# Kernel optimization log

Hardware: AMD Instinct MI355X
Metric: run time of the kernel (lower is better)

The kernel has to match this reference:

```python
import jax, jax.numpy as jnp
import numpy as np

B, S, D = 8, 2048, 512

def setup_inputs() -> dict:
    key = jax.random.key(0)
    ks = jax.random.split(key, 9)
    scale = 1.0 / np.sqrt(D)
    q = jax.random.normal(ks[0], (B, S, D), dtype=jnp.float32)
    k = jax.random.normal(ks[1], (B, S, D), dtype=jnp.float32)
    v = jax.random.normal(ks[2], (B, S, D), dtype=jnp.float32)
    # causal mask, broadcast over batch: True = attend
    mask = jnp.tril(jnp.ones((S, S), dtype=bool))[None, :, :]
    Wq = jax.random.normal(ks[3], (D, D), dtype=jnp.float32) * scale
    bq = jax.random.normal(ks[4], (D,), dtype=jnp.float32) * scale
    Wk = jax.random.normal(ks[5], (D, D), dtype=jnp.float32) * scale
    bk = jax.random.normal(ks[6], (D,), dtype=jnp.float32) * scale
    Wv = jax.random.normal(ks[7], (D, D), dtype=jnp.float32) * scale
    bv = jax.random.normal(ks[8], (D,), dtype=jnp.float32) * scale
    return {"q": q, "k": k, "v": v, "mask": mask,
            "Wq": Wq, "bq": bq, "Wk": Wk, "bk": bk, "Wv": Wv, "bv": bv}

def reference(q, k, v, mask, Wq, bq, Wk, bk, Wv, bv):
    # torch nn.Linear: x @ W^T + b
    Q = jnp.einsum('bsd,ed->bse', q, Wq) + bq
    K = jnp.einsum('bsd,ed->bse', k, Wk) + bk
    V = jnp.einsum('bsd,ed->bse', v, Wv) + bv
    scores = jnp.einsum('bqd,bkd->bqk', Q, K) / jnp.sqrt(jnp.float32(D))
    scores = jnp.where(mask, scores, jnp.float32(-1e9))
    prob = jax.nn.softmax(scores, axis=-1)
    out = jnp.einsum('bqk,bkd->bqd', prob, V)
    return out
```

## Files before the change

### kernel.cpp

```cpp
#include <hip/hip_runtime.h>
#include <stdint.h>
#include <stddef.h>
#include <math.h>

typedef _Float16 half8 __attribute__((ext_vector_type(8)));
typedef float f32x4 __attribute__((ext_vector_type(4)));

#define SCALE_QK 0.04419417382415922f

__device__ __forceinline__ void gload16(const void* g, void* lds) {
  __builtin_amdgcn_global_load_lds(
      (const __attribute__((address_space(1))) void*)g,
      (__attribute__((address_space(3))) void*)lds,
      16, 0, 0);
}

template<bool A_F32>
__device__ __forceinline__ void run_kloop_sb(const void* Arow0, const _Float16* Brow0,
                                             int lda, int ldb, int kIters,
                                             _Float16* As, _Float16* Bs,
                                             f32x4 (&acc)[4][4])
{
  const int tid  = threadIdx.x;
  const int lane = tid & 63;
  const int w    = tid >> 6;
  const int wm   = w >> 1, wn = w & 1;
  const int srow = tid >> 3;
  const int sg   = tid & 7;
  const int swz  = sg ^ (srow & 7);
  const int fr   = lane & 15;
  const int fq   = lane >> 4;
  const int fx   = lane & 7;

  for (int it = 0; it < kIters; ++it) {
    const int k0 = it * 64;
    if constexpr (A_F32) {
      const float* A = (const float*)Arow0;
      f32x4 preF[8];
      #pragma unroll
      for (int i = 0; i < 4; ++i) {
        const float* src = A + (size_t)(i*32 + srow) * lda + (k0 + sg*8);
        preF[2*i]   = *(const f32x4*)src;
        preF[2*i+1] = *(const f32x4*)(src + 4);
      }
      #pragma unroll
      for (int i = 0; i < 4; ++i)
        gload16(Brow0 + (size_t)(i*32 + srow) * ldb + (k0 + swz*8), Bs + i*2048 + w*512);
      #pragma unroll
      for (int i = 0; i < 4; ++i) {
        f32x4 x = preF[2*i], y = preF[2*i+1];
        half8 h;
        h[0]=(_Float16)x[0]; h[1]=(_Float16)x[1]; h[2]=(_Float16)x[2]; h[3]=(_Float16)x[3];
        h[4]=(_Float16)y[0]; h[5]=(_Float16)y[1]; h[6]=(_Float16)y[2]; h[7]=(_Float16)y[3];
        *(half8*)(As + (i*32 + srow)*64 + swz*8) = h;
      }
    } else {
      const _Float16* A = (const _Float16*)Arow0;
      #pragma unroll
      for (int i = 0; i < 4; ++i)
        gload16(A + (size_t)(i*32 + srow) * lda + (k0 + swz*8), As + i*2048 + w*512);
      #pragma unroll
      for (int i = 0; i < 4; ++i)
        gload16(Brow0 + (size_t)(i*32 + srow) * ldb + (k0 + swz*8), Bs + i*2048 + w*512);
    }
    __syncthreads();

    #pragma unroll
    for (int ks = 0; ks < 2; ++ks) {
      half8 av[4], bv[4];
      const int slot = (ks*4 + fq) ^ fx;
      #pragma unroll
      for (int i = 0; i < 4; ++i) {
        av[i] = *(const half8*)(As + (wm*64 + i*16 + fr)*64 + slot*8);
        bv[i] = *(const half8*)(Bs + (wn*64 + i*16 + fr)*64 + slot*8);
      }
      #pragma unroll
      for (int i = 0; i < 4; ++i) {
        #pragma unroll
        for (int j = 0; j < 4; ++j)
          acc[i][j] = __builtin_amdgcn_mfma_f32_16x16x32_f16(av[i], bv[j], acc[i][j], 0, 0, 0);
      }
    }
    __syncthreads();
  }
}

__global__ __launch_bounds__(256) void k_cvtw(const float* __restrict__ Wq,
                                              const float* __restrict__ Wk,
                                              const float* __restrict__ Wv,
                                              _Float16* __restrict__ Wb)
{
  const int t = blockIdx.x * 256 + threadIdx.x;
  const int base = t * 8;
  const int z = base >> 18;
  const int off = base & 262143;
  const float* src = (z == 0) ? Wq : ((z == 1) ? Wk : Wv);
  f32x4 a = *(const f32x4*)(src + off);
  f32x4 b = *(const f32x4*)(src + off + 4);
  half8 h;
  h[0]=(_Float16)a[0]; h[1]=(_Float16)a[1]; h[2]=(_Float16)a[2]; h[3]=(_Float16)a[3];
  h[4]=(_Float16)b[0]; h[5]=(_Float16)b[1]; h[6]=(_Float16)b[2]; h[7]=(_Float16)b[3];
  *(half8*)(Wb + base) = h;
}

__global__ __launch_bounds__(256, 3) void k_proj(const float* __restrict__ q,
                                                 const float* __restrict__ k,
                                                 const float* __restrict__ v,
                                                 const _Float16* __restrict__ Wb,
                                                 const float* __restrict__ bq,
                                                 const float* __restrict__ bk,
                                                 const float* __restrict__ bv,
                                                 _Float16* __restrict__ Qb,
                                                 _Float16* __restrict__ Kb,
                                                 _Float16* __restrict__ Vt)
{
  __shared__ __align__(16) _Float16 LDSbuf[128*132];
  _Float16* As = LDSbuf;
  _Float16* Bs = LDSbuf + 8192;

  const int bid = blockIdx.x;
  const int xcd = bid & 7, i = bid >> 3;
  const int p = xcd * 48 + (i >> 2);
  const int nt = i & 3;
  const int z = p >> 7, mt = p & 127;

  const float* A     = (z == 0) ? q  : (z == 1) ? k  : v;
  const float* bia   = (z == 0) ? bq : (z == 1) ? bk : bv;
  const _Float16* B  = Wb + (size_t)z * 512 * 512;

  f32x4 acc[4][4] = {};
  run_kloop_sb<true>(A + (size_t)mt*128*512, B + (size_t)nt*128*512, 512, 512, 8,
                     As, Bs, acc);

  const int tid = threadIdx.x;
  const int lane = tid & 63, w = tid >> 6;
  const int wm = w >> 1, wn = w & 1;
  const int fr = lane & 15, fq = lane >> 4;

  if (z < 2) {
    _Float16* C = (z == 0) ? Qb : Kb;
    #pragma unroll
    for (int j = 0; j < 4; ++j) {
      const int col = nt*128 + wn*64 + j*16 + fr;
      const float bval = bia[col];
      #pragma unroll
      for (int i2 = 0; i2 < 4; ++i2) {
        const int row = mt*128 + wm*64 + i2*16 + fq*4;
        #pragma unroll
        for (int r = 0; r < 4; ++r)
          C[(size_t)(row + r) * 512 + col] = (_Float16)(acc[i2][j][r] + bval);
      }
    }
  } else {
    _Float16* sm = LDSbuf;
    #pragma unroll
    for (int j = 0; j < 4; ++j) {
      const int colloc = wn*64 + j*16 + fr;
      const float bval = bia[nt*128 + colloc];
      #pragma unroll
      for (int i2 = 0; i2 < 4; ++i2) {
        const int rowloc = wm*64 + i2*16 + fq*4;
        #pragma unroll
        for (int r = 0; r < 4; ++r)
          sm[colloc*132 + rowloc + r] = (_Float16)(acc[i2][j][r] + bval);
      }
    }
    __syncthreads();
    const int bb = mt >> 4, s0 = (mt & 15) * 128;
    #pragma unroll
    for (int q8 = 0; q8 < 8; ++q8) {
      const int dloc = q8*16 + (tid >> 4);
      const int ch   = tid & 15;
      half8 o = *(const half8*)&sm[dloc*132 + ch*8];
      *(half8*)(Vt + ((size_t)bb*512 + nt*128 + dloc)*2048 + s0 + ch*8) = o;
    }
  }
}

__global__ __launch_bounds__(256, 4) void k_scores(const _Float16* __restrict__ Qb,
                                                   const _Float16* __restrict__ Kb,
                                                   _Float16* __restrict__ P)
{
  __shared__ __align__(16) _Float16 As[128*64], Bs[128*64];
  const int bid = blockIdx.x;
  const int b = bid & 7;
  const int t = bid >> 3;
  int qt = (int)((sqrtf(8.0f * (float)t + 1.0f) - 1.0f) * 0.5f);
  int base = (qt * (qt + 1)) >> 1;
  if (t < base)                { --qt; base = (qt * (qt + 1)) >> 1; }
  else if (t >= base + qt + 1) { ++qt; base = (qt * (qt + 1)) >> 1; }
  const int kt = t - base;

  f32x4 acc[4][4] = {};
  run_kloop_sb<false>(Qb + ((size_t)b*2048 + qt*128)*512,
                      Kb + ((size_t)b*2048 + kt*128)*512,
                      512, 512, 8, As, Bs, acc);
  const int lane = threadIdx.x & 63, w = threadIdx.x >> 6;
  const int wm = w >> 1, wn = w & 1;
  const int fr = lane & 15, fq = lane >> 4;
  #pragma unroll
  for (int i = 0; i < 4; ++i) {
    const int row = qt*128 + wm*64 + i*16 + fq*4;
    #pragma unroll
    for (int j = 0; j < 4; ++j) {
      const int col = kt*128 + wn*64 + j*16 + fr;
      #pragma unroll
      for (int r = 0; r < 4; ++r)
        P[((size_t)b*2048 + row + r) * 2048 + col] = (_Float16)(acc[i][j][r] * SCALE_QK);
    }
  }
}

__global__ __launch_bounds__(256) void k_softmax(_Float16* __restrict__ P)
{
  const int lane = threadIdx.x & 63;
  const int row  = blockIdx.x * 4 + (threadIdx.x >> 6);
  const int qIdx = row & 2047;
  _Float16* p = P + (size_t)row * 2048;
  const int L    = qIdx + 1;
  const int Lpad = ((qIdx >> 7) + 1) * 128;

  half8 xb[4];
  float m = -1e30f, s = 0.f;
  #pragma unroll
  for (int c = 0; c < 4; ++c) {
    const int i0 = lane * 8 + c * 512;
    if (i0 < Lpad) {
      half8 x = *(const half8*)(p + i0);
      xb[c] = x;
      float xv[8];
      #pragma unroll
      for (int j = 0; j < 8; ++j) xv[j] = (i0 + j < L) ? (float)x[j] : -1e30f;
      float cm = xv[0];
      #pragma unroll
      for (int j = 1; j < 8; ++j) cm = fmaxf(cm, xv[j]);
      const float mn = fmaxf(m, cm);
      float cs = 0.f;
      #pragma unroll
      for (int j = 0; j < 8; ++j) cs += __expf(xv[j] - mn);
      s = s * __expf(m - mn) + cs;
      m = mn;
    }
  }
  #pragma unroll
  for (int d = 1; d < 64; d <<= 1) {
    const float mo = __shfl_xor(m, d, 64);
    const float so = __shfl_xor(s, d, 64);
    const float mn = fmaxf(m, mo);
    s = s * __expf(m - mn) + so * __expf(mo - mn);
    m = mn;
  }
  const float inv = 1.0f / s;

  #pragma unroll
  for (int c = 0; c < 4; ++c) {
    const int i0 = lane * 8 + c * 512;
    if (i0 < Lpad) {
      half8 x = xb[c];
      half8 o;
      #pragma unroll
      for (int j = 0; j < 8; ++j)
        o[j] = (i0 + j < L) ? (_Float16)(__expf((float)x[j] - m) * inv) : (_Float16)0.f;
      *(half8*)(p + i0) = o;
    }
  }
}

__global__ __launch_bounds__(256, 4) void k_pv(const _Float16* __restrict__ P,
                                               const _Float16* __restrict__ Vt,
                                               float* __restrict__ Out)
{
  __shared__ __align__(16) _Float16 As[128*64], Bs[128*64];
  const int bid = blockIdx.x;
  const int b = bid & 7;
  const int r0 = bid >> 3;
  const int qi = r0 >> 2, dt = r0 & 3;
  const int qt = (qi & 1) ? (15 - (qi >> 1)) : (qi >> 1);

  f32x4 acc[4][4] = {};
  run_kloop_sb<false>(P  + ((size_t)b*2048 + qt*128)*2048,
                      Vt + ((size_t)b*512  + dt*128)*2048,
                      2048, 2048, (qt + 1) * 2, As, Bs, acc);
  const int lane = threadIdx.x & 63, w = threadIdx.x >> 6;
  const int wm = w >> 1, wn = w & 1;
  const int fr = lane & 15, fq = lane >> 4;
  #pragma unroll
  for (int i = 0; i < 4; ++i) {
    const int row = qt*128 + wm*64 + i*16 + fq*4;
    #pragma unroll
    for (int j = 0; j < 4; ++j) {
      const int col = dt*128 + wn*64 + j*16 + fr;
      #pragma unroll
      for (int r = 0; r < 4; ++r)
        Out[((size_t)b*2048 + row + r) * 512 + col] = acc[i][j][r];
    }
  }
}

extern "C" void kernel_launch(void* const* d_in, const int* in_sizes, int n_in,
                              void* d_out, int out_size, void* d_ws, size_t ws_size,
                              hipStream_t stream) {
  (void)in_sizes; (void)n_in; (void)out_size;
  const float* q  = (const float*)d_in[0];
  const float* k  = (const float*)d_in[1];
  const float* v  = (const float*)d_in[2];
  const float* Wq = (const float*)d_in[4];
  const float* bq = (const float*)d_in[5];
  const float* Wk = (const float*)d_in[6];
  const float* bk = (const float*)d_in[7];
  const float* Wv = (const float*)d_in[8];
  const float* bv = (const float*)d_in[9];

  const size_t OFF_P  = 0;
  const size_t OFF_Q  = (size_t)64 << 20;
  const size_t OFF_K  = (size_t)80 << 20;
  const size_t OFF_VT = (size_t)112 << 20;
  const size_t OFF_W  = (size_t)128 << 20;
  const size_t NEEDED = OFF_W + (size_t)3 * 512 * 512 * sizeof(_Float16);
  if (ws_size < NEEDED) return;

  char* ws = (char*)d_ws;
  _Float16* P  = (_Float16*)(ws + OFF_P);
  _Float16* Qb = (_Float16*)(ws + OFF_Q);
  _Float16* Kb = (_Float16*)(ws + OFF_K);
  _Float16* Vt = (_Float16*)(ws + OFF_VT);
  _Float16* Wb = (_Float16*)(ws + OFF_W);
  float* Out = (float*)d_out;

  k_cvtw   <<<dim3(384),  dim3(256), 0, stream>>>(Wq, Wk, Wv, Wb);
  k_proj   <<<dim3(1536), dim3(256), 0, stream>>>(q, k, v, Wb, bq, bk, bv, Qb, Kb, Vt);
  k_scores <<<dim3(1088), dim3(256), 0, stream>>>(Qb, Kb, P);
  k_softmax<<<dim3(4096), dim3(256), 0, stream>>>(P);
  k_pv     <<<dim3(512),  dim3(256), 0, stream>>>(P, Vt, Out);
}
```

Before: 262.7 us.

## Widen projection and score GEMM tiles to 128x256 with per-wave N=128

After: 270.5 us. +3.0%, slower.

```diff
diff --git a/kernel.cpp b/kernel.cpp
--- a/kernel.cpp
+++ b/kernel.cpp
@@ -16,10 +16,10 @@
 }
 
 template<bool A_F32>
-__device__ __forceinline__ void run_kloop_sb(const void* Arow0, const _Float16* Brow0,
-                                             int lda, int ldb, int kIters,
-                                             _Float16* As, _Float16* Bs,
-                                             f32x4 (&acc)[4][4])
+__device__ __forceinline__ void run_kloop_wide(const void* Arow0, const _Float16* Brow0,
+                                               int lda, int ldb, int kIters,
+                                               _Float16* As, _Float16* Bs,
+                                               f32x4 (&acc)[4][8])
 {
   const int tid  = threadIdx.x;
   const int lane = tid & 63;
@@ -44,7 +44,7 @@
         preF[2*i+1] = *(const f32x4*)(src + 4);
       }
       #pragma unroll
-      for (int i = 0; i < 4; ++i)
+      for (int i = 0; i < 8; ++i)
         gload16(Brow0 + (size_t)(i*32 + srow) * ldb + (k0 + swz*8), Bs + i*2048 + w*512);
       #pragma unroll
       for (int i = 0; i < 4; ++i) {
@@ -60,9 +60,56 @@
       for (int i = 0; i < 4; ++i)
         gload16(A + (size_t)(i*32 + srow) * lda + (k0 + swz*8), As + i*2048 + w*512);
       #pragma unroll
+      for (int i = 0; i < 8; ++i)
+        gload16(Brow0 + (size_t)(i*32 + srow) * ldb + (k0 + swz*8), Bs + i*2048 + w*512);
+    }
+    __syncthreads();
+
+    #pragma unroll
+    for (int ks = 0; ks < 2; ++ks) {
+      half8 av[4], bv[8];
+      const int slot = (ks*4 + fq) ^ fx;
+      #pragma unroll
       for (int i = 0; i < 4; ++i)
-        gload16(Brow0 + (size_t)(i*32 + srow) * ldb + (k0 + swz*8), Bs + i*2048 + w*512);
-    }
+        av[i] = *(const half8*)(As + (wm*64 + i*16 + fr)*64 + slot*8);
+      #pragma unroll
+      for (int j = 0; j < 8; ++j)
+        bv[j] = *(const half8*)(Bs + (wn*128 + j*16 + fr)*64 + slot*8);
+      #pragma unroll
+      for (int i = 0; i < 4; ++i) {
+        #pragma unroll
+        for (int j = 0; j < 8; ++j)
+          acc[i][j] = __builtin_amdgcn_mfma_f32_16x16x32_f16(av[i], bv[j], acc[i][j], 0, 0, 0);
+      }
+    }
+    __syncthreads();
+  }
+}
+
+__device__ __forceinline__ void run_kloop_sb(const _Float16* Arow0, const _Float16* Brow0,
+                                             int lda, int ldb, int kIters,
+                                             _Float16* As, _Float16* Bs,
+                                             f32x4 (&acc)[4][4])
+{
+  const int tid  = threadIdx.x;
+  const int lane = tid & 63;
+  const int w    = tid >> 6;
+  const int wm   = w >> 1, wn = w & 1;
+  const int srow = tid >> 3;
+  const int sg   = tid & 7;
+  const int swz  = sg ^ (srow & 7);
+  const int fr   = lane & 15;
+  const int fq   = lane >> 4;
+  const int fx   = lane & 7;
+
+  for (int it = 0; it < kIters; ++it) {
+    const int k0 = it * 64;
+    #pragma unroll
+    for (int i = 0; i < 4; ++i)
+      gload16(Arow0 + (size_t)(i*32 + srow) * lda + (k0 + swz*8), As + i*2048 + w*512);
+    #pragma unroll
+    for (int i = 0; i < 4; ++i)
+      gload16(Brow0 + (size_t)(i*32 + srow) * ldb + (k0 + swz*8), Bs + i*2048 + w*512);
     __syncthreads();
 
     #pragma unroll
@@ -103,7 +150,7 @@
   *(half8*)(Wb + base) = h;
 }
 
-__global__ __launch_bounds__(256, 3) void k_proj(const float* __restrict__ q,
+__global__ __launch_bounds__(256, 2) void k_proj(const float* __restrict__ q,
                                                  const float* __restrict__ k,
                                                  const float* __restrict__ v,
                                                  const _Float16* __restrict__ Wb,
@@ -114,23 +161,23 @@
                                                  _Float16* __restrict__ Kb,
                                                  _Float16* __restrict__ Vt)
 {
-  __shared__ __align__(16) _Float16 LDSbuf[128*132];
+  __shared__ __align__(16) _Float16 LDSbuf[256*132];
   _Float16* As = LDSbuf;
   _Float16* Bs = LDSbuf + 8192;
 
   const int bid = blockIdx.x;
   const int xcd = bid & 7, i = bid >> 3;
-  const int p = xcd * 48 + (i >> 2);
-  const int nt = i & 3;
+  const int p = xcd * 48 + (i >> 1);
+  const int nt2 = i & 1;
   const int z = p >> 7, mt = p & 127;
 
   const float* A     = (z == 0) ? q  : (z == 1) ? k  : v;
   const float* bia   = (z == 0) ? bq : (z == 1) ? bk : bv;
   const _Float16* B  = Wb + (size_t)z * 512 * 512;
 
-  f32x4 acc[4][4] = {};
-  run_kloop_sb<true>(A + (size_t)mt*128*512, B + (size_t)nt*128*512, 512, 512, 8,
-                     As, Bs, acc);
+  f32x4 acc[4][8] = {};
+  run_kloop_wide<true>(A + (size_t)mt*128*512, B + (size_t)nt2*256*512, 512, 512, 8,
+                       As, Bs, acc);
 
   const int tid = threadIdx.x;
   const int lane = tid & 63, w = tid >> 6;
@@ -140,8 +187,8 @@
   if (z < 2) {
     _Float16* C = (z == 0) ? Qb : Kb;
     #pragma unroll
-    for (int j = 0; j < 4; ++j) {
-      const int col = nt*128 + wn*64 + j*16 + fr;
+    for (int j = 0; j < 8; ++j) {
+      const int col = nt2*256 + wn*128 + j*16 + fr;
       const float bval = bia[col];
       #pragma unroll
       for (int i2 = 0; i2 < 4; ++i2) {
@@ -154,9 +201,9 @@
   } else {
     _Float16* sm = LDSbuf;
     #pragma unroll
-    for (int j = 0; j < 4; ++j) {
-      const int colloc = wn*64 + j*16 + fr;
-      const float bval = bia[nt*128 + colloc];
+    for (int j = 0; j < 8; ++j) {
+      const int colloc = wn*128 + j*16 + fr;
+      const float bval = bia[nt2*256 + colloc];
       #pragma unroll
       for (int i2 = 0; i2 < 4; ++i2) {
         const int rowloc = wm*64 + i2*16 + fq*4;
@@ -168,45 +215,53 @@
     __syncthreads();
     const int bb = mt >> 4, s0 = (mt & 15) * 128;
     #pragma unroll
-    for (int q8 = 0; q8 < 8; ++q8) {
+    for (int q8 = 0; q8 < 16; ++q8) {
       const int dloc = q8*16 + (tid >> 4);
       const int ch   = tid & 15;
       half8 o = *(const half8*)&sm[dloc*132 + ch*8];
-      *(half8*)(Vt + ((size_t)bb*512 + nt*128 + dloc)*2048 + s0 + ch*8) = o;
-    }
-  }
-}
-
-__global__ __launch_bounds__(256, 4) void k_scores(const _Float16* __restrict__ Qb,
+      *(half8*)(Vt + ((size_t)bb*512 + nt2*256 + dloc)*2048 + s0 + ch*8) = o;
+    }
+  }
+}
+
+__global__ __launch_bounds__(256, 2) void k_scores(const _Float16* __restrict__ Qb,
                                                    const _Float16* __restrict__ Kb,
                                                    _Float16* __restrict__ P)
 {
-  __shared__ __align__(16) _Float16 As[128*64], Bs[128*64];
+  __shared__ __align__(16) _Float16 As[128*64], Bs[256*64];
   const int bid = blockIdx.x;
   const int b = bid & 7;
-  const int t = bid >> 3;
-  int qt = (int)((sqrtf(8.0f * (float)t + 1.0f) - 1.0f) * 0.5f);
-  int base = (qt * (qt + 1)) >> 1;
-  if (t < base)                { --qt; base = (qt * (qt + 1)) >> 1; }
-  else if (t >= base + qt + 1) { ++qt; base = (qt * (qt + 1)) >> 1; }
-  const int kt = t - base;
-
-  f32x4 acc[4][4] = {};
-  run_kloop_sb<false>(Qb + ((size_t)b*2048 + qt*128)*512,
-                      Kb + ((size_t)b*2048 + kt*128)*512,
-                      512, 512, 8, As, Bs, acc);
+  const int t = 71 - (bid >> 3);
+  int qt = 0, accum = 0;
+  while (accum + (qt >> 1) + 1 <= t) { accum += (qt >> 1) + 1; ++qt; }
+  const int kt0 = (t - accum) * 2;
+
+  f32x4 acc[4][8] = {};
+  run_kloop_wide<false>(Qb + ((size_t)b*2048 + qt*128)*512,
+                        Kb + ((size_t)b*2048 + kt0*128)*512,
+                        512, 512, 8, As, Bs, acc);
+
   const int lane = threadIdx.x & 63, w = threadIdx.x >> 6;
   const int wm = w >> 1, wn = w & 1;
   const int fr = lane & 15, fq = lane >> 4;
-  #pragma unroll
-  for (int i = 0; i < 4; ++i) {
-    const int row = qt*128 + wm*64 + i*16 + fq*4;
-    #pragma unroll
-    for (int j = 0; j < 4; ++j) {
-      const int col = kt*128 + wn*64 + j*16 + fr;
-      #pragma unroll
-      for (int r = 0; r < 4; ++r)
-        P[((size_t)b*2048 + row + r) * 2048 + col] = (_Float16)(acc[i][j][r] * SCALE_QK);
+
+  const int kt = kt0 + wn;
+  if (kt <= qt) {
+    const bool diag = (kt == qt);
+    #pragma unroll
+    for (int i = 0; i < 4; ++i) {
+      const int rl = wm*64 + i*16 + fq*4;
+      #pragma unroll
+      for (int j = 0; j < 8; ++j) {
+        const int cl = j*16 + fr;
+        #pragma unroll
+        for (int r = 0; r < 4; ++r) {
+          const float sc = acc[i][j][r] * SCALE_QK;
+          const bool msk = diag && (cl > rl + r);
+          P[((size_t)b*2048 + qt*128 + rl + r) * 2048 + kt*128 + cl] =
+              msk ? (_Float16)(-30000.0f) : (_Float16)sc;
+        }
+      }
     }
   }
 }
@@ -278,9 +333,9 @@
   const int qt = (qi & 1) ? (15 - (qi >> 1)) : (qi >> 1);
 
   f32x4 acc[4][4] = {};
-  run_kloop_sb<false>(P  + ((size_t)b*2048 + qt*128)*2048,
-                      Vt + ((size_t)b*512  + dt*128)*2048,
-                      2048, 2048, (qt + 1) * 2, As, Bs, acc);
+  run_kloop_sb(P  + ((size_t)b*2048 + qt*128)*2048,
+               Vt + ((size_t)b*512  + dt*128)*2048,
+               2048, 2048, (qt + 1) * 2, As, Bs, acc);
   const int lane = threadIdx.x & 63, w = threadIdx.x >> 6;
   const int wm = w >> 1, wn = w & 1;
   const int fr = lane & 15, fq = lane >> 4;
@@ -328,8 +383,8 @@
   float* Out = (float*)d_out;
 
   k_cvtw   <<<dim3(384),  dim3(256), 0, stream>>>(Wq, Wk, Wv, Wb);
-  k_proj   <<<dim3(1536), dim3(256), 0, stream>>>(q, k, v, Wb, bq, bk, bv, Qb, Kb, Vt);
-  k_scores <<<dim3(1088), dim3(256), 0, stream>>>(Qb, Kb, P);
+  k_proj   <<<dim3(768),  dim3(256), 0, stream>>>(q, k, v, Wb, bq, bk, bv, Qb, Kb, Vt);
+  k_scores <<<dim3(576),  dim3(256), 0, stream>>>(Qb, Kb, P);
   k_softmax<<<dim3(4096), dim3(256), 0, stream>>>(P);
   k_pv     <<<dim3(512),  dim3(256), 0, stream>>>(P, Vt, Out);
 }
```
